# Kernel tuning notes

Measured on AMD Instinct MI355X. Metric: run time of the kernel, lower is better.

Reference implementation:

```python
import jax, jax.numpy as jnp
import numpy as np

B, T0, H0, W0 = 16, 8, 14, 14
DIM = 768
HEADS = 8
HD = DIM // HEADS  # 96
N = T0 * H0 * W0 + 1  # 1569 (cls token)
STRIDE_Q = (1, 1, 1)
STRIDE_KV = (1, 2, 2)
REL_SP_DIM = 2 * max(H0, H0 // 2) - 1  # 27
REL_T_DIM = 2 * T0 - 1  # 15
LN_EPS = 1e-5


def _rel_idx(q, k):
    # decomposed relative-position index table (static, numpy)
    q_ratio = max(k / q, 1.0)
    k_ratio = max(q / k, 1.0)
    d = np.arange(q)[:, None] * q_ratio - np.arange(k)[None, :] * k_ratio
    d += (k - 1) * k_ratio
    return d.astype(np.int64)


def _layernorm(x, g, b):
    m = jnp.mean(x, axis=-1, keepdims=True)
    v = jnp.mean((x - m) ** 2, axis=-1, keepdims=True)
    return (x - m) * jax.lax.rsqrt(v + LN_EPS) * g + b


def _attention_pool(t, w, thw, stride, g, b):
    # t: [B, heads, 1+L, C]; depthwise 3x3x3 conv over THW, cls token bypasses pool
    cls_tok, body = t[:, :, :1], t[:, :, 1:]
    Bb, NH, L, C = body.shape
    T, H, W = thw
    x = body.reshape(Bb * NH, T, H, W, C).transpose(0, 4, 1, 2, 3)  # NCDHW
    y = jax.lax.conv_general_dilated(
        x, w, window_strides=stride, padding=[(1, 1), (1, 1), (1, 1)],
        feature_group_count=C, dimension_numbers=('NCDHW', 'OIDHW', 'NCDHW'))
    nT, nH, nW = y.shape[2], y.shape[3], y.shape[4]
    y = y.reshape(Bb, NH, C, nT * nH * nW).transpose(0, 1, 3, 2)
    y = jnp.concatenate([cls_tok, y], axis=2)
    return _layernorm(y, g, b), (nT, nH, nW)


def setup_inputs() -> dict:
    key = jax.random.key(0)
    ks = jax.random.split(key, 12)
    s = 0.02
    inp = {
        'x': jax.random.normal(ks[0], (B, N, DIM), jnp.float32),
        'qkv_w': jax.random.normal(ks[1], (DIM, 3 * DIM), jnp.float32) * s,
        'qkv_b': jax.random.normal(ks[2], (3 * DIM,), jnp.float32) * s,
        'pool_q_w': jax.random.normal(ks[3], (HD, 1, 3, 3, 3), jnp.float32) * s,
        'pool_k_w': jax.random.normal(ks[4], (HD, 1, 3, 3, 3), jnp.float32) * s,
        'pool_v_w': jax.random.normal(ks[5], (HD, 1, 3, 3, 3), jnp.float32) * s,
        'ln_q_g': jnp.ones((HD,), jnp.float32), 'ln_q_b': jnp.zeros((HD,), jnp.float32),
        'ln_k_g': jnp.ones((HD,), jnp.float32), 'ln_k_b': jnp.zeros((HD,), jnp.float32),
        'ln_v_g': jnp.ones((HD,), jnp.float32), 'ln_v_b': jnp.zeros((HD,), jnp.float32),
        'rel_pos_h': jax.random.normal(ks[6], (REL_SP_DIM, HD), jnp.float32) * s,
        'rel_pos_w': jax.random.normal(ks[7], (REL_SP_DIM, HD), jnp.float32) * s,
        'rel_pos_t': jax.random.normal(ks[8], (REL_T_DIM, HD), jnp.float32) * s,
        'proj_w': jax.random.normal(ks[9], (DIM, DIM), jnp.float32) * s,
        'proj_b': jax.random.normal(ks[10], (DIM,), jnp.float32) * s,
        'thw_t': T0, 'thw_h': H0, 'thw_w': W0,
    }
    return inp


def reference(x, qkv_w, qkv_b, pool_q_w, pool_k_w, pool_v_w,
              ln_q_g, ln_q_b, ln_k_g, ln_k_b, ln_v_g, ln_v_b,
              rel_pos_h, rel_pos_w, rel_pos_t, proj_w, proj_b,
              thw_t, thw_h, thw_w):
    thw = (int(thw_t), int(thw_h), int(thw_w))
    Bb, Nn, _ = x.shape
    qkv = (x @ qkv_w + qkv_b).reshape(Bb, Nn, 3, HEADS, HD).transpose(2, 0, 3, 1, 4)
    q, k, v = qkv[0], qkv[1], qkv[2]  # [B, H, N, hd]
    q, q_shape = _attention_pool(q, pool_q_w, thw, STRIDE_Q, ln_q_g, ln_q_b)
    k, k_shape = _attention_pool(k, pool_k_w, thw, STRIDE_KV, ln_k_g, ln_k_b)
    v, _ = _attention_pool(v, pool_v_w, thw, STRIDE_KV, ln_v_g, ln_v_b)
    qt, qh, qw = q_shape
    kt, kh, kw = k_shape
    scale = HD ** -0.5
    attn = jnp.einsum('bhqc,bhkc->bhqk', q * scale, k)  # [B,H,1+Lq,1+Lk]
    # spatial + temporal decomposed relative position bias (cls row/col excluded)
    Rh = rel_pos_h[_rel_idx(qh, kh)]  # [qh,kh,hd]
    Rw = rel_pos_w[_rel_idx(qw, kw)]  # [qw,kw,hd]
    Rt = rel_pos_t[_rel_idx(qt, kt)]  # [qt,kt,hd]
    r_q = q[:, :, 1:].reshape(Bb, HEADS, qt, qh, qw, HD)
    rel_h = jnp.einsum('bythwc,hkc->bythwk', r_q, Rh)  # [B,H,qt,qh,qw,kh]
    rel_w = jnp.einsum('bythwc,wkc->bythwk', r_q, Rw)  # [B,H,qt,qh,qw,kw]
    rel_t = jnp.einsum('bnthwc,tkc->bnthwk', r_q, Rt)  # [B,H,qt,qh,qw,kt]
    bias = (rel_h[:, :, :, :, :, None, :, None]
            + rel_w[:, :, :, :, :, None, None, :]
            + rel_t[:, :, :, :, :, :, None, None])  # [B,H,qt,qh,qw,kt,kh,kw]
    attn = attn.at[:, :, 1:, 1:].add(bias.reshape(Bb, HEADS, qt * qh * qw, kt * kh * kw))
    attn = jax.nn.softmax(attn, axis=-1)
    out = jnp.einsum('bhqk,bhkc->bhqc', attn, v)
    out = out.at[:, :, 1:].add(q[:, :, 1:])  # residual pooling (skip cls)
    out = out.transpose(0, 2, 1, 3).reshape(Bb, -1, DIM)
    out = out @ proj_w + proj_b
    return out
```

## Files before the change

kernel.cpp:

```cpp
#include <hip/hip_runtime.h>
#include <hip/hip_bf16.h>

typedef __hip_bfloat16 bf16;
typedef __attribute__((ext_vector_type(8))) short bf16x8;
typedef __attribute__((ext_vector_type(4))) float f32x4;

#define B_     16
#define N_     1569
#define DIM_   768
#define NHEADS 8
#define HD_    96
#define LK_    393
#define T0_    8
#define H0_    14
#define W0_    14

struct __align__(8) bf16x4s { bf16 a, b, c, d; };

__device__ __forceinline__ float b2f(unsigned short u) {
  union { unsigned int i; float f; } x;
  x.i = ((unsigned int)u) << 16;
  return x.f;
}

__global__ __launch_bounds__(256) void cvt_f32_bf16(
    const float* __restrict__ in, bf16* __restrict__ out, int n4) {
  int i = blockIdx.x * 256 + threadIdx.x;
  if (i < n4) {
    float4 v = ((const float4*)in)[i];
    bf16x4s o{__float2bfloat16(v.x), __float2bfloat16(v.y),
              __float2bfloat16(v.z), __float2bfloat16(v.w)};
    ((bf16x4s*)out)[i] = o;
  }
}

__global__ __launch_bounds__(256) void transpose_f32_bf16(
    const float* __restrict__ in, bf16* __restrict__ out, int R, int C) {
  __shared__ float tile[32][33];
  int c0 = blockIdx.x * 32, r0 = blockIdx.y * 32;
  int tx = threadIdx.x, ty = threadIdx.y;
  for (int i = 0; i < 32; i += 8) {
    int r = r0 + ty + i, c = c0 + tx;
    if (r < R && c < C) tile[ty + i][tx] = in[(size_t)r * C + c];
  }
  __syncthreads();
  for (int i = 0; i < 32; i += 8) {
    int c = c0 + ty + i, r = r0 + tx;
    if (c < C && r < R) out[(size_t)c * R + r] = __float2bfloat16(tile[tx][ty + i]);
  }
}

__global__ __launch_bounds__(256) void prep_pw(
    const float* __restrict__ wq, const float* __restrict__ wk,
    const float* __restrict__ wv, float* __restrict__ outp) {
  int i = blockIdx.x * 256 + threadIdx.x;
  if (i < 2592) {
    int widx = i / 96, x = i % 96;
    outp[i]        = wq[x * 27 + widx];
    outp[2592 + i] = wk[x * 27 + widx];
    outp[5184 + i] = wv[x * 27 + widx];
  }
}

__device__ __forceinline__ void gl_lds16(const bf16* g, bf16* l) {
  __builtin_amdgcn_global_load_lds(
      (const __attribute__((address_space(1))) void*)g,
      (__attribute__((address_space(3))) void*)l, 16, 0, 0);
}

template <typename OutT>
__global__ __launch_bounds__(256) void gemm_bt(
    const bf16* __restrict__ A, const bf16* __restrict__ BT,
    const float* __restrict__ bias, OutT* __restrict__ C,
    int M, int Nn, int K) {
  constexpr int BM = 128, BN = 128, BK = 64;
  __shared__ __align__(16) char smem[BM * BK * 2 + BN * BK * 2];
  bf16 (*As)[BK] = (bf16(*)[BK])smem;
  bf16 (*Bs)[BK] = (bf16(*)[BK])(smem + BM * BK * 2);
  const int tid = threadIdx.x;
  const int lane = tid & 63, wave = tid >> 6;

  const int nNp = Nn >> 7;
  const int nwg = gridDim.x;
  const int q8 = nwg >> 3, r8 = nwg & 7;
  const int xcd = blockIdx.x & 7, idx = blockIdx.x >> 3;
  const int w = (xcd < r8 ? xcd * (q8 + 1) : r8 * (q8 + 1) + (xcd - r8) * q8) + idx;
  const int bm = (w / nNp) * BM, bn = (w % nNp) * BN;

  const int wm = (wave >> 1) * 64, wn = (wave & 1) * 64;
  const int sl = lane >> 3;
  const int sc = ((lane & 7) ^ sl) * 8;

  f32x4 acc[4][4];
#pragma unroll
  for (int i = 0; i < 4; ++i)
#pragma unroll
    for (int j = 0; j < 4; ++j) acc[i][j] = (f32x4){0.f, 0.f, 0.f, 0.f};

  for (int k0 = 0; k0 < K; k0 += BK) {
#pragma unroll
    for (int c = 0; c < 4; ++c) {
      int r0 = wave * 32 + c * 8;
      int arow = bm + r0 + sl;
      if (arow >= M) arow = M - 1;
      gl_lds16(A + (size_t)arow * K + k0 + sc, &As[r0][0]);
      int brow = bn + r0 + sl;
      gl_lds16(BT + (size_t)brow * K + k0 + sc, &Bs[r0][0]);
    }
    __syncthreads();
    const int fr = lane & 15, q = lane >> 4;
#pragma unroll
    for (int ks = 0; ks < 2; ++ks) {
      const int ph = (((ks << 2) + q) ^ (fr & 7)) << 3;
      bf16x8 af[4], bfr[4];
#pragma unroll
      for (int i = 0; i < 4; ++i) {
        af[i] = *(const bf16x8*)&As[wm + i * 16 + fr][ph];
        bfr[i] = *(const bf16x8*)&Bs[wn + i * 16 + fr][ph];
      }
#pragma unroll
      for (int i = 0; i < 4; ++i)
#pragma unroll
        for (int j = 0; j < 4; ++j)
          acc[i][j] = __builtin_amdgcn_mfma_f32_16x16x32_bf16(af[i], bfr[j],
                                                              acc[i][j], 0, 0, 0);
    }
    __syncthreads();
  }

  const int fr = lane & 15, rg = (lane >> 4) * 4;
  if constexpr (sizeof(OutT) == 2) {
    bf16 (*Cs)[BN] = (bf16(*)[BN])smem;
#pragma unroll
    for (int j = 0; j < 4; ++j) {
      int lc = wn + j * 16 + fr;
      float bv = bias[bn + lc];
#pragma unroll
      for (int i = 0; i < 4; ++i) {
#pragma unroll
        for (int r = 0; r < 4; ++r) {
          int lr = wm + i * 16 + rg + r;
          int pc = lc ^ ((((lr >> 2) & 3)) << 4);
          Cs[lr][pc] = __float2bfloat16(acc[i][j][r] + bv);
        }
      }
    }
    __syncthreads();
#pragma unroll
    for (int k = 0; k < 8; ++k) {
      int c = tid + k * 256;
      int row = c >> 4, seg = c & 15;
      int grow = bm + row;
      int ps = seg ^ (((row >> 2) & 3) << 1);
      if (grow < M)
        *(uint4*)&C[(size_t)grow * Nn + bn + seg * 8] =
            *(const uint4*)&Cs[row][ps * 8];
    }
  } else {
#pragma unroll
    for (int j = 0; j < 4; ++j) {
      int col = bn + wn + j * 16 + fr;
      float bv = bias[col];
#pragma unroll
      for (int i = 0; i < 4; ++i) {
#pragma unroll
        for (int r = 0; r < 4; ++r) {
          int row = bm + wm + i * 16 + rg + r;
          if (row < M)
            C[(size_t)row * Nn + col] = (OutT)(acc[i][j][r] + bv);
        }
      }
    }
  }
}

__global__ __launch_bounds__(256) void pool_ln(
    const bf16* __restrict__ qkv, const float* __restrict__ pwT,
    const float* __restrict__ g, const float* __restrict__ bt,
    bf16* __restrict__ outp, int which, int sHW, int oH, int oW, int Lout) {
  __shared__ float pwl[27 * 104];
  const int tid = threadIdx.x;
  for (int i = tid; i < 2592; i += 256) {
    int widx = i / 96, c = i % 96;
    int cgi = c >> 3, j = c & 7;
    pwl[widx * 104 + cgi * 8 + (cgi >> 2) * 4 + j] = pwT[i];
  }
  __syncthreads();

  const int rloc = tid >> 4;
  const int cg = tid & 15;
  const int orow = blockIdx.x * 16 + rloc;
  if (orow >= Lout) return;
  const int bh = blockIdx.y;
  const int b = bh >> 3, h = bh & 7;
  const bool act = (cg < 12);
  const bf16* base =
      qkv + (size_t)b * N_ * 2304 + which * 768 + h * 96 + cg * 8;

  float acc[8];
#pragma unroll
  for (int j = 0; j < 8; ++j) acc[j] = 0.f;

  if (act) {
    if (orow == 0) {
      union { uint4 u; bf16 e[8]; } tv;
      tv.u = *(const uint4*)base;
#pragma unroll
      for (int j = 0; j < 8; ++j) acc[j] = (float)tv.e[j];
    } else {
      int pos = orow - 1;
      int ot = pos / (oH * oW), r = pos % (oH * oW);
      int oh = r / oW, ow = r % oW;
      const float* wrow = pwl + cg * 8 + (cg >> 2) * 4;
#pragma unroll
      for (int kt = 0; kt < 3; ++kt) {
        int it = ot + kt - 1;
        if (it < 0 || it >= T0_) continue;
#pragma unroll
        for (int kh = 0; kh < 3; ++kh) {
          int ih = oh * sHW + kh - 1;
          if (ih < 0 || ih >= H0_) continue;
#pragma unroll
          for (int kw = 0; kw < 3; ++kw) {
            int iw = ow * sHW + kw - 1;
            if (iw < 0 || iw >= W0_) continue;
            int n = 1 + (it * H0_ + ih) * W0_ + iw;
            int widx = (kt * 3 + kh) * 3 + kw;
            union { uint4 u; bf16 e[8]; } tv;
            tv.u = *(const uint4*)(base + (size_t)n * 2304);
            const float* w = wrow + widx * 104;
            float wv_[8];
            *(float4*)&wv_[0] = *(const float4*)w;
            *(float4*)&wv_[4] = *(const float4*)(w + 4);
#pragma unroll
            for (int j = 0; j < 8; ++j) acc[j] += (float)tv.e[j] * wv_[j];
          }
        }
      }
    }
  }

  float s = 0.f, s2 = 0.f;
#pragma unroll
  for (int j = 0; j < 8; ++j) { s += acc[j]; s2 += acc[j] * acc[j]; }
#pragma unroll
  for (int mk = 1; mk < 16; mk <<= 1) {
    s += __shfl_xor(s, mk);
    s2 += __shfl_xor(s2, mk);
  }
  float mean = s * (1.f / 96.f);
  float var = s2 * (1.f / 96.f) - mean * mean;
  float rstd = rsqrtf(var + 1e-5f);

  if (act) {
    float gv[8], bv[8];
    *(float4*)&gv[0] = *(const float4*)(g + cg * 8);
    *(float4*)&gv[4] = *(const float4*)(g + cg * 8 + 4);
    *(float4*)&bv[0] = *(const float4*)(bt + cg * 8);
    *(float4*)&bv[4] = *(const float4*)(bt + cg * 8 + 4);
    union { uint4 u; bf16 e[8]; } ov;
#pragma unroll
    for (int j = 0; j < 8; ++j)
      ov.e[j] = __float2bfloat16((acc[j] - mean) * rstd * gv[j] + bv[j]);
    *(uint4*)(outp + ((size_t)bh * Lout + orow) * 96 + cg * 8) = ov.u;
  }
}

__global__ __launch_bounds__(256) void vtran(
    const bf16* __restrict__ vp, bf16* __restrict__ vt) {
  __shared__ __align__(16) bf16 tile[64][104];
  const int tid = threadIdx.x;
  const int bh = blockIdx.y, kt0 = blockIdx.x * 64;
  const bf16* src = vp + (size_t)bh * LK_ * HD_;
  for (int c = tid; c < 768; c += 256) {
    int row = c / 12, seg = c % 12;
    int key = kt0 + row;
    uint4 v = {0u, 0u, 0u, 0u};
    if (key < LK_) v = *(const uint4*)(src + (size_t)key * HD_ + seg * 8);
    *(uint4*)&tile[row][seg * 8] = v;
  }
  __syncthreads();
  bf16* dst = vt + (size_t)bh * 96 * 448 + kt0;
  for (int c = tid; c < 768; c += 256) {
    int d = c >> 3, ch = c & 7;
    union { uint4 u; bf16 e[8]; } o;
#pragma unroll
    for (int j = 0; j < 8; ++j) o.e[j] = tile[ch * 8 + j][d];
    *(uint4*)(dst + (size_t)d * 448 + ch * 8) = o.u;
  }
}

__global__ __launch_bounds__(256) void rel_dots(
    const bf16* __restrict__ qp, const float* __restrict__ rpt,
    const float* __restrict__ rph, const float* __restrict__ rpw,
    float* __restrict__ relq) {
  __shared__ float tab[69 * 100];
  __shared__ __align__(16) bf16 Qls[64][96];
  const int tid = threadIdx.x;
  const int bh = blockIdx.y;
  const int q0 = blockIdx.x * 64;
  const bf16* qb = qp + (size_t)bh * N_ * HD_;

  for (int i = tid; i < 69 * 24; i += 256) {
    int row = i / 24, c4 = (i % 24) * 4;
    const float* src = row < 15 ? rpt + row * 96
                      : row < 42 ? rph + (row - 15) * 96
                                 : rpw + (row - 42) * 96;
    *(float4*)&tab[row * 100 + c4] = *(const float4*)(src + c4);
  }
  for (int c = tid; c < 768; c += 256) {
    int row = c / 12, seg = c % 12;
    int p = q0 + row;
    if (p >= N_) p = N_ - 1;
    *(uint4*)&Qls[row][seg * 8] = *(const uint4*)(qb + (size_t)p * HD_ + seg * 8);
  }
  __syncthreads();

  const int r8 = tid >> 5, slot = tid & 31;
  if (slot == 15 || slot >= 23) return;
  for (int g = 0; g < 8; ++g) {
    int row = g * 8 + r8;
    int p = q0 + row;
    if (p < 1 || p >= N_) continue;
    int pos = p - 1;
    int qt = pos / 196, rr = pos % 196;
    int qh = rr / 14, qw = rr % 14;
    int ti = slot < 8 ? qt - slot + 7
            : slot < 15 ? 15 + (qh - 2 * (slot - 8) + 12)
                        : 42 + (qw - 2 * (slot - 16) + 12);
    const float* trow = &tab[ti * 100];
    float acc = 0.f;
#pragma unroll
    for (int d4 = 0; d4 < 24; ++d4) {
      float4 w = *(const float4*)(trow + d4 * 4);
      union { uint2 u; unsigned short s[4]; } qv;
      qv.u = *(const uint2*)&Qls[row][d4 * 4];
      acc += w.x * b2f(qv.s[0]) + w.y * b2f(qv.s[1]) +
             w.z * b2f(qv.s[2]) + w.w * b2f(qv.s[3]);
    }
    relq[((size_t)bh * N_ + p) * 24 + slot] = acc;
  }
}

__global__ __launch_bounds__(256) void attn_fused(
    const bf16* __restrict__ qp, const bf16* __restrict__ kp,
    const bf16* __restrict__ vtb, const float* __restrict__ relq,
    bf16* __restrict__ aout) {
  __shared__ __align__(16) bf16 Ks[64][104];
  __shared__ __align__(16) bf16 VtS[96 * 64];
  __shared__ __align__(16) bf16 Ps[4][16][72];
  __shared__ float relb[64][24];

  const int tid = threadIdx.x;
  const int wv = tid >> 6, lane = tid & 63;
  const int col = lane & 15, quad = lane >> 4;
  const int bh = blockIdx.y;
  const int b = bh >> 3;
  const int h = bh & 7;
  const int q0 = blockIdx.x * 64;
  const bf16* qb = qp + (size_t)bh * N_ * HD_;
  const bf16* kb = kp + (size_t)bh * LK_ * HD_;
  const bf16* vt = vtb + (size_t)bh * 96 * 448;
  const float scale = 0.102062072615966f;

  {
    int nrow = N_ - q0;
    if (nrow > 64) nrow = 64;
    int n4 = nrow * 6;
    const uint4* src = (const uint4*)(relq + ((size_t)bh * N_ + q0) * 24);
    for (int i = tid; i < n4; i += 256) ((uint4*)relb)[i] = src[i];
  }

  int qrow = q0 + wv * 16 + col;
  if (qrow >= N_) qrow = N_ - 1;
  bf16x8 qa[3];
#pragma unroll
  for (int ks_ = 0; ks_ < 3; ++ks_)
    qa[ks_] = *(const bf16x8*)(qb + (size_t)qrow * HD_ + ks_ * 32 + quad * 8);

  int krow[3], kseg[3];
  int voff[3];
  bf16* vdst[3];
#pragma unroll
  for (int i = 0; i < 3; ++i) {
    int c = tid + i * 256;
    krow[i] = c / 12;
    kseg[i] = (c % 12) * 8;
    int ci = wv * 192 + i * 64 + lane;
    int d = ci >> 3, j0 = (ci & 7) * 8;
    int c_ = (d ^ (d >> 3)) & 7;
    voff[i] = d * 448 + (j0 ^ (c_ * 8));
    vdst[i] = (bf16*)VtS + (size_t)(wv * 192 + i * 64) * 8;
  }

  float mrun[4] = {-1e30f, -1e30f, -1e30f, -1e30f};
  float lrun[4] = {0.f, 0.f, 0.f, 0.f};
  f32x4 oacc[6];
#pragma unroll
  for (int dt = 0; dt < 6; ++dt) oacc[dt] = (f32x4){0.f, 0.f, 0.f, 0.f};

  for (int kt_i = 0; kt_i < 7; ++kt_i) {
    const int kt0 = kt_i * 64;
    __syncthreads();
#pragma unroll
    for (int i = 0; i < 3; ++i) {
      int key = kt0 + krow[i];
      if (key >= LK_) key = LK_ - 1;
      *(uint4*)&Ks[krow[i]][kseg[i]] =
          *(const uint4*)(kb + (size_t)key * HD_ + kseg[i]);
      gl_lds16(vt + voff[i] + kt0, vdst[i]);
    }
    __syncthreads();

    f32x4 sacc[4];
#pragma unroll
    for (int jt = 0; jt < 4; ++jt) sacc[jt] = (f32x4){0.f, 0.f, 0.f, 0.f};
#pragma unroll
    for (int ks_ = 0; ks_ < 3; ++ks_) {
#pragma unroll
      for (int jt = 0; jt < 4; ++jt) {
        bf16x8 bk = *(const bf16x8*)&Ks[jt * 16 + col][ks_ * 32 + quad * 8];
        sacc[jt] = __builtin_amdgcn_mfma_f32_16x16x32_bf16(qa[ks_], bk, sacc[jt], 0, 0, 0);
      }
    }

    float sv[4][4];
#pragma unroll
    for (int jt = 0; jt < 4; ++jt) {
      int kglob = kt0 + jt * 16 + col;
      bool kvalid = (kglob < LK_);
      int kbod = (kglob >= 1) ? kglob - 1 : 0;
      int kt_ = kbod / 49, krem = kbod % 49;
      int kh_ = krem / 7, kw_ = krem % 7;
#pragma unroll
      for (int r = 0; r < 4; ++r) {
        int qr = wv * 16 + quad * 4 + r;
        int p = q0 + qr;
        float s = sacc[jt][r] * scale;
        if (kvalid && kglob >= 1 && p >= 1 && p < N_)
          s += relb[qr][kt_] + relb[qr][8 + kh_] + relb[qr][16 + kw_];
        if (!kvalid) s = -1e30f;
        sv[jt][r] = s;
      }
    }

    float pexp[4][4];
#pragma unroll
    for (int r = 0; r < 4; ++r) {
      float pm = fmaxf(fmaxf(sv[0][r], sv[1][r]), fmaxf(sv[2][r], sv[3][r]));
#pragma unroll
      for (int mk = 1; mk < 16; mk <<= 1) pm = fmaxf(pm, __shfl_xor(pm, mk));
      float mn = fmaxf(mrun[r], pm);
      float alpha = __expf(mrun[r] - mn);
      mrun[r] = mn;
      float rs = 0.f;
#pragma unroll
      for (int jt = 0; jt < 4; ++jt) {
        float e = __expf(sv[jt][r] - mn);
        pexp[jt][r] = e;
        rs += e;
      }
#pragma unroll
      for (int mk = 1; mk < 16; mk <<= 1) rs += __shfl_xor(rs, mk);
      lrun[r] = lrun[r] * alpha + rs;
#pragma unroll
      for (int dt = 0; dt < 6; ++dt) {
        oacc[dt][r] *= alpha;
      }
    }

#pragma unroll
    for (int jt = 0; jt < 4; ++jt)
#pragma unroll
      for (int r = 0; r < 4; ++r)
        Ps[wv][quad * 4 + r][jt * 16 + col] = __float2bfloat16(pexp[jt][r]);

#pragma unroll
    for (int ks_ = 0; ks_ < 2; ++ks_) {
      bf16x8 ap = *(const bf16x8*)&Ps[wv][col][ks_ * 32 + quad * 8];
#pragma unroll
      for (int dt = 0; dt < 6; ++dt) {
        int d = dt * 16 + col;
        int c_ = (d ^ (d >> 3)) & 7;
        bf16x8 bv =
            *(const bf16x8*)&VtS[d * 64 + ((ks_ * 32 + quad * 8) ^ (c_ << 3))];
        oacc[dt] = __builtin_amdgcn_mfma_f32_16x16x32_bf16(ap, bv, oacc[dt], 0, 0, 0);
      }
    }
  }

#pragma unroll
  for (int r = 0; r < 4; ++r) {
    int qr = wv * 16 + quad * 4 + r;
    int p = q0 + qr;
    if (p >= N_) continue;
    float inv = 1.f / lrun[r];
#pragma unroll
    for (int dt = 0; dt < 6; ++dt) {
      int d = dt * 16 + col;
      float val = oacc[dt][r] * inv;
      if (p >= 1) val += (float)qb[(size_t)p * HD_ + d];
      aout[((size_t)b * N_ + p) * DIM_ + h * HD_ + d] = __float2bfloat16(val);
    }
  }
}

extern "C" void kernel_launch(void* const* d_in, const int* in_sizes, int n_in,
                              void* d_out, int out_size, void* d_ws,
                              size_t ws_size, hipStream_t stream) {
  (void)in_sizes; (void)n_in; (void)out_size; (void)ws_size;
  const float* x      = (const float*)d_in[0];
  const float* qkv_w  = (const float*)d_in[1];
  const float* qkv_b  = (const float*)d_in[2];
  const float* pool_q = (const float*)d_in[3];
  const float* pool_k = (const float*)d_in[4];
  const float* pool_v = (const float*)d_in[5];
  const float* ln_q_g = (const float*)d_in[6];
  const float* ln_q_b = (const float*)d_in[7];
  const float* ln_k_g = (const float*)d_in[8];
  const float* ln_k_b = (const float*)d_in[9];
  const float* ln_v_g = (const float*)d_in[10];
  const float* ln_v_b = (const float*)d_in[11];
  const float* rph    = (const float*)d_in[12];
  const float* rpw    = (const float*)d_in[13];
  const float* rpt    = (const float*)d_in[14];
  const float* proj_w = (const float*)d_in[15];
  const float* proj_b = (const float*)d_in[16];

  char* ws = (char*)d_ws;
  bf16* wt_qkv  = (bf16*)(ws);
  bf16* wt_proj = (bf16*)(ws + 3538944);
  bf16* xb      = (bf16*)(ws + 4718592);
  bf16* aout    = xb;
  bf16* qkv     = (bf16*)(ws + 43278336);
  float* relq   = (float*)(ws + 43278336);
  bf16* vtb     = (bf16*)(ws + 63278336);
  bf16* qpoolb  = (bf16*)(ws + 158957568);
  bf16* kpoolb  = (bf16*)(ws + 197517312);
  bf16* vpoolb  = (bf16*)(ws + 207175680);
  float* pwT    = (float*)(ws + 216834048);
  float* outp   = (float*)d_out;

  int n4 = (B_ * N_ * DIM_) / 4;
  cvt_f32_bf16<<<(n4 + 255) / 256, 256, 0, stream>>>(x, xb, n4);
  transpose_f32_bf16<<<dim3(72, 24), dim3(32, 8), 0, stream>>>(qkv_w, wt_qkv, 768, 2304);
  transpose_f32_bf16<<<dim3(24, 24), dim3(32, 8), 0, stream>>>(proj_w, wt_proj, 768, 768);
  prep_pw<<<11, 256, 0, stream>>>(pool_q, pool_k, pool_v, pwT);

  gemm_bt<bf16><<<197 * 18, 256, 0, stream>>>(xb, wt_qkv, qkv_b, qkv,
                                              B_ * N_, 3 * DIM_, DIM_);

  pool_ln<<<dim3(99, 128), 256, 0, stream>>>(qkv, pwT, ln_q_g, ln_q_b, qpoolb,
                                             0, 1, 14, 14, N_);
  pool_ln<<<dim3(25, 128), 256, 0, stream>>>(qkv, pwT + 2592, ln_k_g, ln_k_b,
                                             kpoolb, 1, 2, 7, 7, LK_);
  pool_ln<<<dim3(25, 128), 256, 0, stream>>>(qkv, pwT + 5184, ln_v_g, ln_v_b,
                                             vpoolb, 2, 2, 7, 7, LK_);

  vtran<<<dim3(7, 128), 256, 0, stream>>>(vpoolb, vtb);
  rel_dots<<<dim3(25, 128), 256, 0, stream>>>(qpoolb, rpt, rph, rpw, relq);

  attn_fused<<<dim3(25, 128), 256, 0, stream>>>(qpoolb, kpoolb, vtb, relq,
                                                aout);

  gemm_bt<float><<<197 * 6, 256, 0, stream>>>(aout, wt_proj, proj_b, outp,
                                              B_ * N_, DIM_, DIM_);
}
```

Measured before the change: 706.9 us.

## Fold rel-pos bias into MFMA via indicator matrix and register-prefetch K/V tiles

The decomposed relative-position bias is no longer added with per-element scalar LDS lookups. It is computed as an extra MFMA: relq values (bf16, pre-scaled by 1/scale into 32 padded slots) are multiplied by a precomputed one-hot indicator matrix over keys. K and V tiles are prefetched into registers during the PV step and written to LDS at the end of each iteration, replacing load-then-sync at the top of each loop. An XOR swizzle on the P buffer reduces bank conflicts. Storing the bias in bf16 loses some precision, and the extra register pressure may lower occupancy.

```diff
diff --git a/kernel.cpp b/kernel.cpp
--- a/kernel.cpp
+++ b/kernel.cpp
@@ -52,13 +52,26 @@
 
 __global__ __launch_bounds__(256) void prep_pw(
     const float* __restrict__ wq, const float* __restrict__ wk,
-    const float* __restrict__ wv, float* __restrict__ outp) {
+    const float* __restrict__ wv, float* __restrict__ outp,
+    bf16* __restrict__ ind) {
   int i = blockIdx.x * 256 + threadIdx.x;
   if (i < 2592) {
     int widx = i / 96, x = i % 96;
     outp[i]        = wq[x * 27 + widx];
     outp[2592 + i] = wk[x * 27 + widx];
     outp[5184 + i] = wv[x * 27 + widx];
+  }
+  if (i < 14336) {
+    int t = i >> 11, r = i & 2047, key = r >> 5, slot = r & 31;
+    int kglob = t * 64 + key;
+    float v = 0.f;
+    if (kglob >= 1 && kglob < LK_) {
+      int kbod = kglob - 1;
+      int kt_ = kbod / 49, krem = kbod % 49;
+      int kh_ = krem / 7, kw_ = krem % 7;
+      if (slot == kt_ || slot == 8 + kh_ || slot == 16 + kw_) v = 1.f;
+    }
+    ind[i] = __float2bfloat16(v);
   }
 }
 
@@ -293,7 +306,7 @@
 __global__ __launch_bounds__(256) void rel_dots(
     const bf16* __restrict__ qp, const float* __restrict__ rpt,
     const float* __restrict__ rph, const float* __restrict__ rpw,
-    float* __restrict__ relq) {
+    bf16* __restrict__ relq2) {
   __shared__ float tab[69 * 100];
   __shared__ __align__(16) bf16 Qls[64][96];
   const int tid = threadIdx.x;
@@ -317,39 +330,41 @@
   __syncthreads();
 
   const int r8 = tid >> 5, slot = tid & 31;
-  if (slot == 15 || slot >= 23) return;
+  const bool slot_ok = !(slot == 15 || slot >= 23);
   for (int g = 0; g < 8; ++g) {
     int row = g * 8 + r8;
     int p = q0 + row;
-    if (p < 1 || p >= N_) continue;
-    int pos = p - 1;
-    int qt = pos / 196, rr = pos % 196;
-    int qh = rr / 14, qw = rr % 14;
-    int ti = slot < 8 ? qt - slot + 7
-            : slot < 15 ? 15 + (qh - 2 * (slot - 8) + 12)
-                        : 42 + (qw - 2 * (slot - 16) + 12);
-    const float* trow = &tab[ti * 100];
     float acc = 0.f;
-#pragma unroll
-    for (int d4 = 0; d4 < 24; ++d4) {
-      float4 w = *(const float4*)(trow + d4 * 4);
-      union { uint2 u; unsigned short s[4]; } qv;
-      qv.u = *(const uint2*)&Qls[row][d4 * 4];
-      acc += w.x * b2f(qv.s[0]) + w.y * b2f(qv.s[1]) +
-             w.z * b2f(qv.s[2]) + w.w * b2f(qv.s[3]);
-    }
-    relq[((size_t)bh * N_ + p) * 24 + slot] = acc;
+    if (slot_ok && p >= 1 && p < N_) {
+      int pos = p - 1;
+      int qt = pos / 196, rr = pos % 196;
+      int qh = rr / 14, qw = rr % 14;
+      int ti = slot < 8 ? qt - slot + 7
+              : slot < 15 ? 15 + (qh - 2 * (slot - 8) + 12)
+                          : 42 + (qw - 2 * (slot - 16) + 12);
+      const float* trow = &tab[ti * 100];
+#pragma unroll
+      for (int d4 = 0; d4 < 24; ++d4) {
+        float4 w = *(const float4*)(trow + d4 * 4);
+        union { uint2 u; unsigned short s[4]; } qv;
+        qv.u = *(const uint2*)&Qls[row][d4 * 4];
+        acc += w.x * b2f(qv.s[0]) + w.y * b2f(qv.s[1]) +
+               w.z * b2f(qv.s[2]) + w.w * b2f(qv.s[3]);
+      }
+    }
+    relq2[((size_t)bh * 1600 + p) * 32 + slot] =
+        __float2bfloat16(acc * 9.7979589711f);
   }
 }
 
 __global__ __launch_bounds__(256) void attn_fused(
     const bf16* __restrict__ qp, const bf16* __restrict__ kp,
-    const bf16* __restrict__ vtb, const float* __restrict__ relq,
-    bf16* __restrict__ aout) {
+    const bf16* __restrict__ vtb, const bf16* __restrict__ relq2,
+    const bf16* __restrict__ indg, bf16* __restrict__ aout) {
   __shared__ __align__(16) bf16 Ks[64][104];
   __shared__ __align__(16) bf16 VtS[96 * 64];
   __shared__ __align__(16) bf16 Ps[4][16][72];
-  __shared__ float relb[64][24];
+  __shared__ __align__(16) bf16 relb2[64][32];
 
   const int tid = threadIdx.x;
   const int wv = tid >> 6, lane = tid & 63;
@@ -364,11 +379,10 @@
   const float scale = 0.102062072615966f;
 
   {
-    int nrow = N_ - q0;
-    if (nrow > 64) nrow = 64;
-    int n4 = nrow * 6;
-    const uint4* src = (const uint4*)(relq + ((size_t)bh * N_ + q0) * 24);
-    for (int i = tid; i < n4; i += 256) ((uint4*)relb)[i] = src[i];
+    int row = tid >> 2, q4 = tid & 3;
+    const uint4* src =
+        (const uint4*)(relq2 + ((size_t)bh * 1600 + q0 + row) * 32);
+    ((uint4*)&relb2[row][0])[q4] = src[q4];
   }
 
   int qrow = q0 + wv * 16 + col;
@@ -380,7 +394,7 @@
 
   int krow[3], kseg[3];
   int voff[3];
-  bf16* vdst[3];
+  int vdst[3];
 #pragma unroll
   for (int i = 0; i < 3; ++i) {
     int c = tid + i * 256;
@@ -390,8 +404,24 @@
     int d = ci >> 3, j0 = (ci & 7) * 8;
     int c_ = (d ^ (d >> 3)) & 7;
     voff[i] = d * 448 + (j0 ^ (c_ * 8));
-    vdst[i] = (bf16*)VtS + (size_t)(wv * 192 + i * 64) * 8;
-  }
+    vdst[i] = ci * 8;
+  }
+
+  uint4 kreg[3], vreg[3];
+#pragma unroll
+  for (int i = 0; i < 3; ++i) {
+    int key = krow[i];
+    kreg[i] = *(const uint4*)(kb + (size_t)key * HD_ + kseg[i]);
+    vreg[i] = *(const uint4*)(vt + voff[i]);
+  }
+#pragma unroll
+  for (int i = 0; i < 3; ++i) {
+    *(uint4*)&Ks[krow[i]][kseg[i]] = kreg[i];
+    *(uint4*)&VtS[vdst[i]] = vreg[i];
+  }
+  __syncthreads();
+
+  const bf16x8 relA = *(const bf16x8*)&relb2[wv * 16 + col][quad * 8];
 
   float mrun[4] = {-1e30f, -1e30f, -1e30f, -1e30f};
   float lrun[4] = {0.f, 0.f, 0.f, 0.f};
@@ -401,16 +431,12 @@
 
   for (int kt_i = 0; kt_i < 7; ++kt_i) {
     const int kt0 = kt_i * 64;
-    __syncthreads();
-#pragma unroll
-    for (int i = 0; i < 3; ++i) {
-      int key = kt0 + krow[i];
-      if (key >= LK_) key = LK_ - 1;
-      *(uint4*)&Ks[krow[i]][kseg[i]] =
-          *(const uint4*)(kb + (size_t)key * HD_ + kseg[i]);
-      gl_lds16(vt + voff[i] + kt0, vdst[i]);
-    }
-    __syncthreads();
+
+    bf16x8 indf[4];
+#pragma unroll
+    for (int jt = 0; jt < 4; ++jt)
+      indf[jt] = *(const bf16x8*)(indg + kt_i * 2048 +
+                                  (jt * 16 + col) * 32 + quad * 8);
 
     f32x4 sacc[4];
 #pragma unroll
@@ -423,24 +449,22 @@
         sacc[jt] = __builtin_amdgcn_mfma_f32_16x16x32_bf16(qa[ks_], bk, sacc[jt], 0, 0, 0);
       }
     }
+#pragma unroll
+    for (int jt = 0; jt < 4; ++jt)
+      sacc[jt] = __builtin_amdgcn_mfma_f32_16x16x32_bf16(relA, indf[jt], sacc[jt], 0, 0, 0);
 
     float sv[4][4];
 #pragma unroll
-    for (int jt = 0; jt < 4; ++jt) {
-      int kglob = kt0 + jt * 16 + col;
-      bool kvalid = (kglob < LK_);
-      int kbod = (kglob >= 1) ? kglob - 1 : 0;
-      int kt_ = kbod / 49, krem = kbod % 49;
-      int kh_ = krem / 7, kw_ = krem % 7;
-#pragma unroll
-      for (int r = 0; r < 4; ++r) {
-        int qr = wv * 16 + quad * 4 + r;
-        int p = q0 + qr;
-        float s = sacc[jt][r] * scale;
-        if (kvalid && kglob >= 1 && p >= 1 && p < N_)
-          s += relb[qr][kt_] + relb[qr][8 + kh_] + relb[qr][16 + kw_];
-        if (!kvalid) s = -1e30f;
-        sv[jt][r] = s;
+    for (int jt = 0; jt < 4; ++jt)
+#pragma unroll
+      for (int r = 0; r < 4; ++r) sv[jt][r] = sacc[jt][r] * scale;
+    if (kt_i == 6) {
+#pragma unroll
+      for (int jt = 0; jt < 4; ++jt) {
+        if (kt0 + jt * 16 + col >= LK_) {
+#pragma unroll
+          for (int r = 0; r < 4; ++r) sv[jt][r] = -1e30f;
+        }
       }
     }
 
@@ -473,11 +497,24 @@
     for (int jt = 0; jt < 4; ++jt)
 #pragma unroll
       for (int r = 0; r < 4; ++r)
-        Ps[wv][quad * 4 + r][jt * 16 + col] = __float2bfloat16(pexp[jt][r]);
+        Ps[wv][quad * 4 + r][(jt * 16 + col) ^ ((quad & 2) << 3)] =
+            __float2bfloat16(pexp[jt][r]);
+
+    if (kt_i < 6) {
+      const int ktn = kt0 + 64;
+#pragma unroll
+      for (int i = 0; i < 3; ++i) {
+        int key = ktn + krow[i];
+        if (key >= LK_) key = LK_ - 1;
+        kreg[i] = *(const uint4*)(kb + (size_t)key * HD_ + kseg[i]);
+        vreg[i] = *(const uint4*)(vt + voff[i] + ktn);
+      }
+    }
 
 #pragma unroll
     for (int ks_ = 0; ks_ < 2; ++ks_) {
-      bf16x8 ap = *(const bf16x8*)&Ps[wv][col][ks_ * 32 + quad * 8];
+      bf16x8 ap = *(const bf16x8*)&Ps[wv][col]
+          [(ks_ * 32 + quad * 8) ^ ((col & 8) << 1)];
 #pragma unroll
       for (int dt = 0; dt < 6; ++dt) {
         int d = dt * 16 + col;
@@ -486,6 +523,16 @@
             *(const bf16x8*)&VtS[d * 64 + ((ks_ * 32 + quad * 8) ^ (c_ << 3))];
         oacc[dt] = __builtin_amdgcn_mfma_f32_16x16x32_bf16(ap, bv, oacc[dt], 0, 0, 0);
       }
+    }
+
+    if (kt_i < 6) {
+      __syncthreads();
+#pragma unroll
+      for (int i = 0; i < 3; ++i) {
+        *(uint4*)&Ks[krow[i]][kseg[i]] = kreg[i];
+        *(uint4*)&VtS[vdst[i]] = vreg[i];
+      }
+      __syncthreads();
     }
   }
 
@@ -533,19 +580,20 @@
   bf16* xb      = (bf16*)(ws + 4718592);
   bf16* aout    = xb;
   bf16* qkv     = (bf16*)(ws + 43278336);
-  float* relq   = (float*)(ws + 43278336);
+  bf16* relq2   = (bf16*)(ws + 43278336);
   bf16* vtb     = (bf16*)(ws + 63278336);
   bf16* qpoolb  = (bf16*)(ws + 158957568);
   bf16* kpoolb  = (bf16*)(ws + 197517312);
   bf16* vpoolb  = (bf16*)(ws + 207175680);
   float* pwT    = (float*)(ws + 216834048);
+  bf16* indb    = (bf16*)(ws + 216865152);
   float* outp   = (float*)d_out;
 
   int n4 = (B_ * N_ * DIM_) / 4;
   cvt_f32_bf16<<<(n4 + 255) / 256, 256, 0, stream>>>(x, xb, n4);
   transpose_f32_bf16<<<dim3(72, 24), dim3(32, 8), 0, stream>>>(qkv_w, wt_qkv, 768, 2304);
   transpose_f32_bf16<<<dim3(24, 24), dim3(32, 8), 0, stream>>>(proj_w, wt_proj, 768, 768);
-  prep_pw<<<11, 256, 0, stream>>>(pool_q, pool_k, pool_v, pwT);
+  prep_pw<<<56, 256, 0, stream>>>(pool_q, pool_k, pool_v, pwT, indb);
 
   gemm_bt<bf16><<<197 * 18, 256, 0, stream>>>(xb, wt_qkv, qkv_b, qkv,
                                               B_ * N_, 3 * DIM_, DIM_);
@@ -558,10 +606,10 @@
                                              vpoolb, 2, 2, 7, 7, LK_);
 
   vtran<<<dim3(7, 128), 256, 0, stream>>>(vpoolb, vtb);
-  rel_dots<<<dim3(25, 128), 256, 0, stream>>>(qpoolb, rpt, rph, rpw, relq);
-
-  attn_fused<<<dim3(25, 128), 256, 0, stream>>>(qpoolb, kpoolb, vtb, relq,
-                                                aout);
+  rel_dots<<<dim3(25, 128), 256, 0, stream>>>(qpoolb, rpt, rph, rpw, relq2);
+
+  attn_fused<<<dim3(25, 128), 256, 0, stream>>>(qpoolb, kpoolb, vtb, relq2,
+                                                indb, aout);
 
   gemm_bt<float><<<197 * 6, 256, 0, stream>>>(aout, wt_proj, proj_b, outp,
                                               B_ * N_, DIM_, DIM_);
```

After: 782.6 us. 1.11x slower.
